# Kernel optimization log

Hardware: AMD Instinct MI355X
Metric: run time of the kernel (lower is better)

Reference implementation:

```python
import jax, jax.numpy as jnp
import numpy as np


def setup_inputs() -> dict:
    key = jax.random.key(0)
    k1, k2, k3 = jax.random.split(key, 3)
    B, N, D = 32, 1024, 256  # batch, seq len (shared), window_len
    t = jax.random.normal(k1, (B, N, D), dtype=jnp.float32)
    f = jax.random.normal(k2, (B, N, D), dtype=jnp.float32)
    W = jax.random.normal(k3, (D, D), dtype=jnp.float32)  # nn.init.normal_(std=1)
    return {"t": t, "f": f, "W": W}


def reference(t, f, W):
    # s_weight[b,n,m] = t[b,n,:] @ W @ f[b,m,:]
    tW = jnp.einsum('bnd,de->bne', t, W)          # [B,N,D]
    s_weight = jnp.einsum('bne,bme->bnm', tW, f)  # [B,N,N]
    t_weight = jax.nn.softmax(s_weight, axis=1)   # softmax over L_t (dim=1)
    f_weight = jax.nn.softmax(s_weight, axis=2)   # softmax over L_f (dim=2)
    # t_out = t^T @ t_weight -> [B,D,N]
    t_out = jnp.einsum('bnd,bnm->bdm', t, t_weight)
    # f_out = f^T @ f_weight -> [B,D,N] (requires L_t == L_f)
    f_out = jnp.einsum('bmd,bmk->bdk', f, f_weight)
    # Dropout(0.3) omitted (eval-mode identity) for deterministic reference.
    return (t_out, f_out)
```

## Files before the change

kernel.cpp:

```cpp
#include <hip/hip_runtime.h>
#include <math.h>

#define BB 32
#define NN 1024
#define DD 256
#define KSTEP 32
#define LDK 40

typedef __attribute__((ext_vector_type(8))) short short8;
typedef __attribute__((ext_vector_type(8))) unsigned short u16x8;
typedef __attribute__((ext_vector_type(4))) float f32x4;

__device__ __forceinline__ unsigned short f2bf(float x) {
  unsigned u = __float_as_uint(x);
  return (unsigned short)((u + 0x7fffu + ((u >> 16) & 1u)) >> 16);
}
__device__ __forceinline__ unsigned short f2bf_fast(float x) {
  return (unsigned short)((__float_as_uint(x) + 0x8000u) >> 16);
}
__device__ __forceinline__ float bf2f(unsigned short h) {
  return __uint_as_float((unsigned)h << 16);
}

__global__ __launch_bounds__(256) void k_split(const float* __restrict__ src,
                                               unsigned short* __restrict__ hi,
                                               unsigned short* __restrict__ lo, int n4) {
  int i = blockIdx.x * 256 + threadIdx.x;
  if (i >= n4) return;
  float4 v = ((const float4*)src)[i];
  float xs[4] = {v.x, v.y, v.z, v.w};
  ushort4 h4, l4;
  unsigned short* hp = (unsigned short*)&h4;
  unsigned short* lp = (unsigned short*)&l4;
  #pragma unroll
  for (int j = 0; j < 4; ++j) {
    unsigned short h = f2bf(xs[j]);
    hp[j] = h;
    lp[j] = f2bf(xs[j] - bf2f(h));
  }
  ((ushort4*)hi)[i] = h4;
  ((ushort4*)lo)[i] = l4;
}

__global__ __launch_bounds__(256) void k_splitW(const float* __restrict__ W,
                                                unsigned short* __restrict__ Wth,
                                                unsigned short* __restrict__ Wtl) {
  int k = blockIdx.x, n = threadIdx.x;
  float x = W[k * DD + n];
  unsigned short h = f2bf(x);
  Wth[n * DD + k] = h;
  Wtl[n * DD + k] = f2bf(x - bf2f(h));
}

__global__ __launch_bounds__(256) void k_transT(const unsigned short* __restrict__ in,
                                                unsigned short* __restrict__ out) {
  const int b = blockIdx.z;
  const int n0 = blockIdx.x * 64, d0 = blockIdx.y * 64;
  const int tid = threadIdx.x;
  const int nl = tid & 63, dc = tid >> 6;
  #pragma unroll
  for (int dj = 0; dj < 16; ++dj) {
    int d = d0 + dc * 16 + dj;
    unsigned short v = in[((size_t)b * NN + n0 + nl) * DD + d];
    out[((size_t)b * DD + d) * NN + n0 + nl] = v;
  }
}

template <int EPI>
__global__ __launch_bounds__(256) void k_gemm_nt(const unsigned short* __restrict__ Ahg,
                                                 const unsigned short* __restrict__ Alg,
                                                 const unsigned short* __restrict__ Bhg,
                                                 const unsigned short* __restrict__ Blg,
                                                 unsigned short* __restrict__ outh,
                                                 unsigned short* __restrict__ outl,
                                                 float* __restrict__ outf,
                                                 float2* __restrict__ prow,
                                                 float2* __restrict__ pcol, int b0) {
  size_t aoff = 0, boff = 0, coff = 0;
  const int g = blockIdx.z;
  if (EPI == 1) {
    int b = b0 + g;
    aoff = (size_t)b * NN * DD;
    boff = (size_t)b * NN * DD;
    coff = (size_t)g * NN * NN;
  }
  const int n0 = blockIdx.x * 128, m0 = blockIdx.y * 128;
  __shared__ unsigned short Ah[128][LDK], Al[128][LDK], Bh[128][LDK], Bl[128][LDK];
  const int tid = threadIdx.x;
  const int lane = tid & 63, w = tid >> 6;
  const int wr = (w >> 1) * 64, wc = (w & 1) * 64;
  const int sr = tid >> 1, sk = (tid & 1) * 16;

  f32x4 acc[4][4] = {};
  const int fr = lane & 15, fk = (lane >> 4) * 8;

  for (int k0 = 0; k0 < DD; k0 += KSTEP) {
    const size_t abase = aoff + (size_t)(n0 + sr) * DD + k0 + sk;
    const size_t bbase = boff + (size_t)(m0 + sr) * DD + k0 + sk;
    *(u16x8*)&Ah[sr][sk] = *(const u16x8*)&Ahg[abase];
    *(u16x8*)&Ah[sr][sk + 8] = *(const u16x8*)&Ahg[abase + 8];
    *(u16x8*)&Al[sr][sk] = *(const u16x8*)&Alg[abase];
    *(u16x8*)&Al[sr][sk + 8] = *(const u16x8*)&Alg[abase + 8];
    *(u16x8*)&Bh[sr][sk] = *(const u16x8*)&Bhg[bbase];
    *(u16x8*)&Bh[sr][sk + 8] = *(const u16x8*)&Bhg[bbase + 8];
    *(u16x8*)&Bl[sr][sk] = *(const u16x8*)&Blg[bbase];
    *(u16x8*)&Bl[sr][sk + 8] = *(const u16x8*)&Blg[bbase + 8];
    __syncthreads();
    short8 ah[4], al[4], bh[4], bl[4];
    #pragma unroll
    for (int mi = 0; mi < 4; ++mi) {
      ah[mi] = *(const short8*)&Ah[wr + mi * 16 + fr][fk];
      al[mi] = *(const short8*)&Al[wr + mi * 16 + fr][fk];
    }
    #pragma unroll
    for (int ni = 0; ni < 4; ++ni) {
      bh[ni] = *(const short8*)&Bh[wc + ni * 16 + fr][fk];
      bl[ni] = *(const short8*)&Bl[wc + ni * 16 + fr][fk];
    }
    #pragma unroll
    for (int mi = 0; mi < 4; ++mi)
      #pragma unroll
      for (int ni = 0; ni < 4; ++ni) {
        acc[mi][ni] = __builtin_amdgcn_mfma_f32_16x16x32_bf16(ah[mi], bh[ni], acc[mi][ni], 0, 0, 0);
        acc[mi][ni] = __builtin_amdgcn_mfma_f32_16x16x32_bf16(ah[mi], bl[ni], acc[mi][ni], 0, 0, 0);
        acc[mi][ni] = __builtin_amdgcn_mfma_f32_16x16x32_bf16(al[mi], bh[ni], acc[mi][ni], 0, 0, 0);
      }
    __syncthreads();
  }
  const int fq = (lane >> 4) * 4;
  if (EPI == 0) {
    #pragma unroll
    for (int mi = 0; mi < 4; ++mi)
      #pragma unroll
      for (int ni = 0; ni < 4; ++ni)
        #pragma unroll
        for (int q = 0; q < 4; ++q) {
          int row = n0 + wr + mi * 16 + fq + q;
          int col = m0 + wc + ni * 16 + fr;
          float x = acc[mi][ni][q];
          unsigned short h = f2bf(x);
          outh[(size_t)row * 256 + col] = h;
          outl[(size_t)row * 256 + col] = f2bf(x - bf2f(h));
        }
  } else {
    #pragma unroll
    for (int mi = 0; mi < 4; ++mi)
      #pragma unroll
      for (int ni = 0; ni < 4; ++ni) {
        int colm = m0 + wc + ni * 16 + fr;
        int nbase = n0 + wr + mi * 16 + fq;
        float4 v = {acc[mi][ni][0], acc[mi][ni][1], acc[mi][ni][2], acc[mi][ni][3]};
        *(float4*)&outf[coff + (size_t)colm * NN + nbase] = v;
      }
    float2 (*rowbuf)[2] = (float2(*)[2])&Ah[0][0];
    float2 (*colbuf)[2] = (float2(*)[2])&Bh[0][0];
    #pragma unroll
    for (int mi = 0; mi < 4; ++mi)
      #pragma unroll
      for (int q = 0; q < 4; ++q) {
        float v0 = acc[mi][0][q], v1 = acc[mi][1][q], v2 = acc[mi][2][q], v3 = acc[mi][3][q];
        float mx = fmaxf(fmaxf(v0, v1), fmaxf(v2, v3));
        #pragma unroll
        for (int mask = 1; mask <= 8; mask <<= 1) mx = fmaxf(mx, __shfl_xor(mx, mask));
        float se = __expf(v0 - mx) + __expf(v1 - mx) + __expf(v2 - mx) + __expf(v3 - mx);
        #pragma unroll
        for (int mask = 1; mask <= 8; mask <<= 1) se += __shfl_xor(se, mask);
        if (fr == 0) rowbuf[wr + mi * 16 + fq + q][w & 1] = make_float2(mx, se);
      }
    #pragma unroll
    for (int ni = 0; ni < 4; ++ni) {
      float mx = -INFINITY;
      #pragma unroll
      for (int mi = 0; mi < 4; ++mi)
        #pragma unroll
        for (int q = 0; q < 4; ++q) mx = fmaxf(mx, acc[mi][ni][q]);
      mx = fmaxf(mx, __shfl_xor(mx, 16));
      mx = fmaxf(mx, __shfl_xor(mx, 32));
      float se = 0.f;
      #pragma unroll
      for (int mi = 0; mi < 4; ++mi)
        #pragma unroll
        for (int q = 0; q < 4; ++q) se += __expf(acc[mi][ni][q] - mx);
      se += __shfl_xor(se, 16);
      se += __shfl_xor(se, 32);
      if ((lane >> 4) == 0) colbuf[wc + ni * 16 + fr][w >> 1] = make_float2(mx, se);
    }
    __syncthreads();
    if (tid < 128) {
      float2 a = rowbuf[tid][0], c = rowbuf[tid][1];
      float nm = fmaxf(a.x, c.x);
      float s = a.y * __expf(a.x - nm) + c.y * __expf(c.x - nm);
      prow[((size_t)g * NN + n0 + tid) * 8 + blockIdx.y] = make_float2(nm, s);
    } else {
      int m = tid - 128;
      float2 a = colbuf[m][0], c = colbuf[m][1];
      float nm = fmaxf(a.x, c.x);
      float s = a.y * __expf(a.x - nm) + c.y * __expf(c.x - nm);
      pcol[((size_t)g * NN + m0 + m) * 8 + blockIdx.x] = make_float2(nm, s);
    }
  }
}

__global__ __launch_bounds__(256) void k_comb(const float2* __restrict__ part,
                                              float* __restrict__ lse, int b0) {
  const int g = blockIdx.y, b = b0 + g;
  const int i = blockIdx.x * 256 + threadIdx.x;
  float mx = -INFINITY, sum = 0.f;
  #pragma unroll
  for (int c = 0; c < 8; ++c) {
    float2 p = part[((size_t)g * NN + i) * 8 + c];
    float nm = fmaxf(mx, p.x);
    sum = sum * __expf(mx - nm) + p.y * __expf(p.x - nm);
    mx = nm;
  }
  lse[(size_t)b * NN + i] = mx + __logf(sum);
}

__global__ __launch_bounds__(256) void k_outdual(const unsigned short* __restrict__ tTg,
                                                 const unsigned short* __restrict__ fTg,
                                                 const float* __restrict__ sT,
                                                 const float* __restrict__ lr,
                                                 const float* __restrict__ lc,
                                                 float* __restrict__ out_t,
                                                 float* __restrict__ out_f, int b0) {
  const int g = blockIdx.z, b = b0 + g;
  const int c0 = blockIdx.x * 64;
  const int d0 = blockIdx.y * 128;
  const unsigned short* At = tTg + (size_t)b * DD * NN;
  const unsigned short* Af = fTg + (size_t)b * DD * NN;
  const float* S = sT + (size_t)g * NN * NN;
  __shared__ unsigned short Ats[128][LDK], Afs[128][LDK];
  __shared__ unsigned short P1s[64][LDK], P2s[64][LDK];
  const int tid = threadIdx.x;
  const int lane = tid & 63, w = tid >> 6;
  const int wd = (w >> 1) * 64, wcc = (w & 1) * 32;
  const int fr = lane & 15, fk = (lane >> 4) * 8, fq = (lane >> 4) * 4;
  const int ar = tid >> 1, ak = (tid & 1) * 16;
  const int srow = tid >> 2, soff = (tid & 3) * 8;
  const float lcv = lc[(size_t)b * NN + c0 + srow];
  f32x4 acc1[4][2] = {}, acc2[4][2] = {};
  for (int r0 = 0; r0 < NN; r0 += KSTEP) {
    const size_t arow = (size_t)(d0 + ar) * NN + r0 + ak;
    u16x8 a_t0 = *(const u16x8*)&At[arow];
    u16x8 a_t1 = *(const u16x8*)&At[arow + 8];
    u16x8 a_f0 = *(const u16x8*)&Af[arow];
    u16x8 a_f1 = *(const u16x8*)&Af[arow + 8];
    float4 v0 = *(const float4*)&S[(size_t)(c0 + srow) * NN + r0 + soff];
    float4 v1 = *(const float4*)&S[(size_t)(c0 + srow) * NN + r0 + soff + 4];
    float4 l0 = *(const float4*)&lr[(size_t)b * NN + r0 + soff];
    float4 l1 = *(const float4*)&lr[(size_t)b * NN + r0 + soff + 4];
    float sv[8] = {v0.x, v0.y, v0.z, v0.w, v1.x, v1.y, v1.z, v1.w};
    float lv[8] = {l0.x, l0.y, l0.z, l0.w, l1.x, l1.y, l1.z, l1.w};
    u16x8 p1, p2;
    #pragma unroll
    for (int j = 0; j < 8; ++j) {
      p1[j] = f2bf_fast(__expf(sv[j] - lcv));
      p2[j] = f2bf_fast(__expf(sv[j] - lv[j]));
    }
    __syncthreads();
    *(u16x8*)&Ats[ar][ak] = a_t0;
    *(u16x8*)&Ats[ar][ak + 8] = a_t1;
    *(u16x8*)&Afs[ar][ak] = a_f0;
    *(u16x8*)&Afs[ar][ak + 8] = a_f1;
    *(u16x8*)&P1s[srow][soff] = p1;
    *(u16x8*)&P2s[srow][soff] = p2;
    __syncthreads();
    short8 at[4], af[4], b1[2], b2[2];
    #pragma unroll
    for (int mi = 0; mi < 4; ++mi) {
      at[mi] = *(const short8*)&Ats[wd + mi * 16 + fr][fk];
      af[mi] = *(const short8*)&Afs[wd + mi * 16 + fr][fk];
    }
    #pragma unroll
    for (int ci = 0; ci < 2; ++ci) {
      b1[ci] = *(const short8*)&P1s[wcc + ci * 16 + fr][fk];
      b2[ci] = *(const short8*)&P2s[wcc + ci * 16 + fr][fk];
    }
    #pragma unroll
    for (int mi = 0; mi < 4; ++mi)
      #pragma unroll
      for (int ci = 0; ci < 2; ++ci) {
        acc1[mi][ci] = __builtin_amdgcn_mfma_f32_16x16x32_bf16(at[mi], b1[ci], acc1[mi][ci], 0, 0, 0);
        acc2[mi][ci] = __builtin_amdgcn_mfma_f32_16x16x32_bf16(af[mi], b2[ci], acc2[mi][ci], 0, 0, 0);
      }
  }
  float* Ot = out_t + (size_t)b * DD * NN;
  float* Of = out_f + (size_t)b * DD * NN;
  #pragma unroll
  for (int mi = 0; mi < 4; ++mi)
    #pragma unroll
    for (int ci = 0; ci < 2; ++ci)
      #pragma unroll
      for (int q = 0; q < 4; ++q) {
        int d = d0 + wd + mi * 16 + fq + q;
        int c = c0 + wcc + ci * 16 + fr;
        Ot[(size_t)d * NN + c] = acc1[mi][ci][q];
        Of[(size_t)d * NN + c] = acc2[mi][ci][q];
      }
}

extern "C" void kernel_launch(void* const* d_in, const int* in_sizes, int n_in,
                              void* d_out, int out_size, void* d_ws, size_t ws_size,
                              hipStream_t stream) {
  const float* t = (const float*)d_in[0];
  const float* f = (const float*)d_in[1];
  const float* W = (const float*)d_in[2];
  float* out = (float*)d_out;

  const size_t NE = (size_t)BB * NN * DD;
  char* ws = (char*)d_ws;
  size_t off = 0;
  auto alloc = [&](size_t bytes) { char* p = ws + off; off += (bytes + 255) & ~(size_t)255; return p; };
  unsigned short* f_hi = (unsigned short*)alloc(NE * 2);
  unsigned short* f_lo = (unsigned short*)alloc(NE * 2);
  unsigned short* tw_hi = (unsigned short*)alloc(NE * 2);
  unsigned short* tw_lo = (unsigned short*)alloc(NE * 2);
  unsigned short* tT = (unsigned short*)alloc(NE * 2);
  unsigned short* fT = (unsigned short*)alloc(NE * 2);
  unsigned short* Wth = (unsigned short*)alloc((size_t)DD * DD * 2);
  unsigned short* Wtl = (unsigned short*)alloc((size_t)DD * DD * 2);
  float* lr = (float*)alloc((size_t)BB * NN * 4);
  float* lc = (float*)alloc((size_t)BB * NN * 4);
  float2* prow = (float2*)alloc((size_t)BB * NN * 8 * 8);
  float2* pcol = (float2*)alloc((size_t)BB * NN * 8 * 8);
  size_t fixed_bytes = off;
  float* sbuf = (float*)(ws + fixed_bytes);
  unsigned short* t_hi = (unsigned short*)(ws + fixed_bytes);
  unsigned short* t_lo = t_hi + NE;
  size_t per_batch = (size_t)NN * NN * 4;
  int G = 1;
  if (ws_size > fixed_bytes + per_batch) {
    size_t avail = (ws_size - fixed_bytes) / per_batch;
    G = (int)(avail < BB ? avail : BB);
    if (G < 1) G = 1;
  }

  float* out_t = out;
  float* out_f = out + (size_t)BB * DD * NN;

  k_split<<<(int)((NE / 4 + 255) / 256), 256, 0, stream>>>(t, t_hi, t_lo, (int)(NE / 4));
  k_split<<<(int)((NE / 4 + 255) / 256), 256, 0, stream>>>(f, f_hi, f_lo, (int)(NE / 4));
  k_splitW<<<DD, DD, 0, stream>>>(W, Wth, Wtl);
  k_transT<<<dim3(NN / 64, DD / 64, BB), 256, 0, stream>>>(t_hi, tT);
  k_transT<<<dim3(NN / 64, DD / 64, BB), 256, 0, stream>>>(f_hi, fT);
  k_gemm_nt<0><<<dim3(256, 2, 1), 256, 0, stream>>>(t_hi, t_lo, Wth, Wtl, tw_hi, tw_lo,
                                                    nullptr, nullptr, nullptr, 0);

  for (int b0 = 0; b0 < BB; b0 += G) {
    int g = BB - b0 < G ? BB - b0 : G;
    k_gemm_nt<1><<<dim3(8, 8, g), 256, 0, stream>>>(tw_hi, tw_lo, f_hi, f_lo, nullptr, nullptr,
                                                    sbuf, prow, pcol, b0);
    k_comb<<<dim3(NN / 256, g), 256, 0, stream>>>(prow, lr, b0);
    k_comb<<<dim3(NN / 256, g), 256, 0, stream>>>(pcol, lc, b0);
    k_outdual<<<dim3(NN / 64, DD / 128, g), 256, 0, stream>>>(tT, fT, sbuf, lr, lc,
                                                              out_t, out_f, b0);
  }
}
```

Measured before the change: 368.3 us.

## Move softmax stats to separate kernel and widen outdual column tile to 128

Removes the fused row/column max-sum epilogue from the score GEMM and adds a standalone k_stats kernel that rereads the fp32 score matrix in 64x64 tiles to produce 16 partials per row and column, combined by k_comb16. Separately, k_outdual's column tile doubles from 64 to 128, so each block computes a 128x128 output with twice the accumulators. That halves how often the t/f transposed operands are reloaded per score column. The cost is an extra full read of the score buffer and higher register pressure in k_outdual, which may lower occupancy.

```diff
diff --git a/kernel.cpp b/kernel.cpp
--- a/kernel.cpp
+++ b/kernel.cpp
@@ -73,9 +73,7 @@
                                                  const unsigned short* __restrict__ Blg,
                                                  unsigned short* __restrict__ outh,
                                                  unsigned short* __restrict__ outl,
-                                                 float* __restrict__ outf,
-                                                 float2* __restrict__ prow,
-                                                 float2* __restrict__ pcol, int b0) {
+                                                 float* __restrict__ outf, int b0) {
   size_t aoff = 0, boff = 0, coff = 0;
   const int g = blockIdx.z;
   if (EPI == 1) {
@@ -152,63 +150,70 @@
         float4 v = {acc[mi][ni][0], acc[mi][ni][1], acc[mi][ni][2], acc[mi][ni][3]};
         *(float4*)&outf[coff + (size_t)colm * NN + nbase] = v;
       }
-    float2 (*rowbuf)[2] = (float2(*)[2])&Ah[0][0];
-    float2 (*colbuf)[2] = (float2(*)[2])&Bh[0][0];
-    #pragma unroll
-    for (int mi = 0; mi < 4; ++mi)
-      #pragma unroll
-      for (int q = 0; q < 4; ++q) {
-        float v0 = acc[mi][0][q], v1 = acc[mi][1][q], v2 = acc[mi][2][q], v3 = acc[mi][3][q];
-        float mx = fmaxf(fmaxf(v0, v1), fmaxf(v2, v3));
-        #pragma unroll
-        for (int mask = 1; mask <= 8; mask <<= 1) mx = fmaxf(mx, __shfl_xor(mx, mask));
-        float se = __expf(v0 - mx) + __expf(v1 - mx) + __expf(v2 - mx) + __expf(v3 - mx);
-        #pragma unroll
-        for (int mask = 1; mask <= 8; mask <<= 1) se += __shfl_xor(se, mask);
-        if (fr == 0) rowbuf[wr + mi * 16 + fq + q][w & 1] = make_float2(mx, se);
-      }
-    #pragma unroll
-    for (int ni = 0; ni < 4; ++ni) {
-      float mx = -INFINITY;
-      #pragma unroll
-      for (int mi = 0; mi < 4; ++mi)
-        #pragma unroll
-        for (int q = 0; q < 4; ++q) mx = fmaxf(mx, acc[mi][ni][q]);
-      mx = fmaxf(mx, __shfl_xor(mx, 16));
-      mx = fmaxf(mx, __shfl_xor(mx, 32));
-      float se = 0.f;
-      #pragma unroll
-      for (int mi = 0; mi < 4; ++mi)
-        #pragma unroll
-        for (int q = 0; q < 4; ++q) se += __expf(acc[mi][ni][q] - mx);
-      se += __shfl_xor(se, 16);
-      se += __shfl_xor(se, 32);
-      if ((lane >> 4) == 0) colbuf[wc + ni * 16 + fr][w >> 1] = make_float2(mx, se);
-    }
-    __syncthreads();
-    if (tid < 128) {
-      float2 a = rowbuf[tid][0], c = rowbuf[tid][1];
-      float nm = fmaxf(a.x, c.x);
-      float s = a.y * __expf(a.x - nm) + c.y * __expf(c.x - nm);
-      prow[((size_t)g * NN + n0 + tid) * 8 + blockIdx.y] = make_float2(nm, s);
-    } else {
-      int m = tid - 128;
-      float2 a = colbuf[m][0], c = colbuf[m][1];
-      float nm = fmaxf(a.x, c.x);
-      float s = a.y * __expf(a.x - nm) + c.y * __expf(c.x - nm);
-      pcol[((size_t)g * NN + m0 + m) * 8 + blockIdx.x] = make_float2(nm, s);
-    }
-  }
-}
-
-__global__ __launch_bounds__(256) void k_comb(const float2* __restrict__ part,
-                                              float* __restrict__ lse, int b0) {
+  }
+}
+
+__global__ __launch_bounds__(256) void k_stats(const float* __restrict__ sT,
+                                               float2* __restrict__ prow,
+                                               float2* __restrict__ pcol) {
+  const int g = blockIdx.z;
+  const int c0 = blockIdx.x * 64, r0 = blockIdx.y * 64;
+  const float* S = sT + (size_t)g * NN * NN;
+  __shared__ float Ls[64][65];
+  const int tid = threadIdx.x;
+  const int row = tid >> 4, c4 = (tid & 15) * 4;
+  #pragma unroll
+  for (int rr = 0; rr < 4; ++rr) {
+    int c = row + rr * 16;
+    *(float4*)&Ls[c][c4] = *(const float4*)&S[(size_t)(c0 + c) * NN + r0 + c4];
+  }
+  __syncthreads();
+  {
+    const int c = tid >> 2, seg = (tid & 3) * 16;
+    float mx = -INFINITY;
+    #pragma unroll
+    for (int j = 0; j < 16; ++j) mx = fmaxf(mx, Ls[c][seg + j]);
+    float se = 0.f;
+    #pragma unroll
+    for (int j = 0; j < 16; ++j) se += __expf(Ls[c][seg + j] - mx);
+    #pragma unroll
+    for (int mask = 1; mask <= 2; mask <<= 1) {
+      float m2 = __shfl_xor(mx, mask), s2 = __shfl_xor(se, mask);
+      float nm = fmaxf(mx, m2);
+      se = se * __expf(mx - nm) + s2 * __expf(m2 - nm);
+      mx = nm;
+    }
+    if ((tid & 3) == 0)
+      pcol[((size_t)g * NN + c0 + c) * 16 + blockIdx.y] = make_float2(mx, se);
+  }
+  {
+    const int r = tid >> 2, seg = (tid & 3) * 16;
+    float mx = -INFINITY;
+    #pragma unroll
+    for (int j = 0; j < 16; ++j) mx = fmaxf(mx, Ls[seg + j][r]);
+    float se = 0.f;
+    #pragma unroll
+    for (int j = 0; j < 16; ++j) se += __expf(Ls[seg + j][r] - mx);
+    #pragma unroll
+    for (int mask = 1; mask <= 2; mask <<= 1) {
+      float m2 = __shfl_xor(mx, mask), s2 = __shfl_xor(se, mask);
+      float nm = fmaxf(mx, m2);
+      se = se * __expf(mx - nm) + s2 * __expf(m2 - nm);
+      mx = nm;
+    }
+    if ((tid & 3) == 0)
+      prow[((size_t)g * NN + r0 + r) * 16 + blockIdx.x] = make_float2(mx, se);
+  }
+}
+
+__global__ __launch_bounds__(256) void k_comb16(const float2* __restrict__ part,
+                                                float* __restrict__ lse, int b0) {
   const int g = blockIdx.y, b = b0 + g;
   const int i = blockIdx.x * 256 + threadIdx.x;
   float mx = -INFINITY, sum = 0.f;
   #pragma unroll
-  for (int c = 0; c < 8; ++c) {
-    float2 p = part[((size_t)g * NN + i) * 8 + c];
+  for (int c = 0; c < 16; ++c) {
+    float2 p = part[((size_t)g * NN + i) * 16 + c];
     float nm = fmaxf(mx, p.x);
     sum = sum * __expf(mx - nm) + p.y * __expf(p.x - nm);
     mx = nm;
@@ -224,62 +229,71 @@
                                                  float* __restrict__ out_t,
                                                  float* __restrict__ out_f, int b0) {
   const int g = blockIdx.z, b = b0 + g;
-  const int c0 = blockIdx.x * 64;
+  const int c0 = blockIdx.x * 128;
   const int d0 = blockIdx.y * 128;
   const unsigned short* At = tTg + (size_t)b * DD * NN;
   const unsigned short* Af = fTg + (size_t)b * DD * NN;
   const float* S = sT + (size_t)g * NN * NN;
   __shared__ unsigned short Ats[128][LDK], Afs[128][LDK];
-  __shared__ unsigned short P1s[64][LDK], P2s[64][LDK];
+  __shared__ unsigned short P1s[128][LDK], P2s[128][LDK];
   const int tid = threadIdx.x;
   const int lane = tid & 63, w = tid >> 6;
-  const int wd = (w >> 1) * 64, wcc = (w & 1) * 32;
+  const int wd = (w >> 1) * 64, wcc = (w & 1) * 64;
   const int fr = lane & 15, fk = (lane >> 4) * 8, fq = (lane >> 4) * 4;
   const int ar = tid >> 1, ak = (tid & 1) * 16;
-  const int srow = tid >> 2, soff = (tid & 3) * 8;
-  const float lcv = lc[(size_t)b * NN + c0 + srow];
-  f32x4 acc1[4][2] = {}, acc2[4][2] = {};
+  const float lcv = lc[(size_t)b * NN + c0 + ar];
+  f32x4 acc1[4][4] = {}, acc2[4][4] = {};
   for (int r0 = 0; r0 < NN; r0 += KSTEP) {
     const size_t arow = (size_t)(d0 + ar) * NN + r0 + ak;
     u16x8 a_t0 = *(const u16x8*)&At[arow];
     u16x8 a_t1 = *(const u16x8*)&At[arow + 8];
     u16x8 a_f0 = *(const u16x8*)&Af[arow];
     u16x8 a_f1 = *(const u16x8*)&Af[arow + 8];
-    float4 v0 = *(const float4*)&S[(size_t)(c0 + srow) * NN + r0 + soff];
-    float4 v1 = *(const float4*)&S[(size_t)(c0 + srow) * NN + r0 + soff + 4];
-    float4 l0 = *(const float4*)&lr[(size_t)b * NN + r0 + soff];
-    float4 l1 = *(const float4*)&lr[(size_t)b * NN + r0 + soff + 4];
-    float sv[8] = {v0.x, v0.y, v0.z, v0.w, v1.x, v1.y, v1.z, v1.w};
-    float lv[8] = {l0.x, l0.y, l0.z, l0.w, l1.x, l1.y, l1.z, l1.w};
-    u16x8 p1, p2;
+    float4 v0 = *(const float4*)&S[(size_t)(c0 + ar) * NN + r0 + ak];
+    float4 v1 = *(const float4*)&S[(size_t)(c0 + ar) * NN + r0 + ak + 4];
+    float4 v2 = *(const float4*)&S[(size_t)(c0 + ar) * NN + r0 + ak + 8];
+    float4 v3 = *(const float4*)&S[(size_t)(c0 + ar) * NN + r0 + ak + 12];
+    float4 l0 = *(const float4*)&lr[(size_t)b * NN + r0 + ak];
+    float4 l1 = *(const float4*)&lr[(size_t)b * NN + r0 + ak + 4];
+    float4 l2 = *(const float4*)&lr[(size_t)b * NN + r0 + ak + 8];
+    float4 l3 = *(const float4*)&lr[(size_t)b * NN + r0 + ak + 12];
+    float sv[16] = {v0.x, v0.y, v0.z, v0.w, v1.x, v1.y, v1.z, v1.w,
+                    v2.x, v2.y, v2.z, v2.w, v3.x, v3.y, v3.z, v3.w};
+    float lv[16] = {l0.x, l0.y, l0.z, l0.w, l1.x, l1.y, l1.z, l1.w,
+                    l2.x, l2.y, l2.z, l2.w, l3.x, l3.y, l3.z, l3.w};
+    u16x8 p1a, p1b, p2a, p2b;
     #pragma unroll
     for (int j = 0; j < 8; ++j) {
-      p1[j] = f2bf_fast(__expf(sv[j] - lcv));
-      p2[j] = f2bf_fast(__expf(sv[j] - lv[j]));
+      p1a[j] = f2bf_fast(__expf(sv[j] - lcv));
+      p2a[j] = f2bf_fast(__expf(sv[j] - lv[j]));
+      p1b[j] = f2bf_fast(__expf(sv[j + 8] - lcv));
+      p2b[j] = f2bf_fast(__expf(sv[j + 8] - lv[j + 8]));
     }
     __syncthreads();
     *(u16x8*)&Ats[ar][ak] = a_t0;
     *(u16x8*)&Ats[ar][ak + 8] = a_t1;
     *(u16x8*)&Afs[ar][ak] = a_f0;
     *(u16x8*)&Afs[ar][ak + 8] = a_f1;
-    *(u16x8*)&P1s[srow][soff] = p1;
-    *(u16x8*)&P2s[srow][soff] = p2;
+    *(u16x8*)&P1s[ar][ak] = p1a;
+    *(u16x8*)&P1s[ar][ak + 8] = p1b;
+    *(u16x8*)&P2s[ar][ak] = p2a;
+    *(u16x8*)&P2s[ar][ak + 8] = p2b;
     __syncthreads();
-    short8 at[4], af[4], b1[2], b2[2];
+    short8 at[4], af[4], b1[4], b2[4];
     #pragma unroll
     for (int mi = 0; mi < 4; ++mi) {
       at[mi] = *(const short8*)&Ats[wd + mi * 16 + fr][fk];
       af[mi] = *(const short8*)&Afs[wd + mi * 16 + fr][fk];
     }
     #pragma unroll
-    for (int ci = 0; ci < 2; ++ci) {
+    for (int ci = 0; ci < 4; ++ci) {
       b1[ci] = *(const short8*)&P1s[wcc + ci * 16 + fr][fk];
       b2[ci] = *(const short8*)&P2s[wcc + ci * 16 + fr][fk];
     }
     #pragma unroll
     for (int mi = 0; mi < 4; ++mi)
       #pragma unroll
-      for (int ci = 0; ci < 2; ++ci) {
+      for (int ci = 0; ci < 4; ++ci) {
         acc1[mi][ci] = __builtin_amdgcn_mfma_f32_16x16x32_bf16(at[mi], b1[ci], acc1[mi][ci], 0, 0, 0);
         acc2[mi][ci] = __builtin_amdgcn_mfma_f32_16x16x32_bf16(af[mi], b2[ci], acc2[mi][ci], 0, 0, 0);
       }
@@ -289,7 +303,7 @@
   #pragma unroll
   for (int mi = 0; mi < 4; ++mi)
     #pragma unroll
-    for (int ci = 0; ci < 2; ++ci)
+    for (int ci = 0; ci < 4; ++ci)
       #pragma unroll
       for (int q = 0; q < 4; ++q) {
         int d = d0 + wd + mi * 16 + fq + q;
@@ -321,8 +335,8 @@
   unsigned short* Wtl = (unsigned short*)alloc((size_t)DD * DD * 2);
   float* lr = (float*)alloc((size_t)BB * NN * 4);
   float* lc = (float*)alloc((size_t)BB * NN * 4);
-  float2* prow = (float2*)alloc((size_t)BB * NN * 8 * 8);
-  float2* pcol = (float2*)alloc((size_t)BB * NN * 8 * 8);
+  float2* prow = (float2*)alloc((size_t)BB * NN * 16 * 8);
+  float2* pcol = (float2*)alloc((size_t)BB * NN * 16 * 8);
   size_t fixed_bytes = off;
   float* sbuf = (float*)(ws + fixed_bytes);
   unsigned short* t_hi = (unsigned short*)(ws + fixed_bytes);
@@ -344,15 +358,16 @@
   k_transT<<<dim3(NN / 64, DD / 64, BB), 256, 0, stream>>>(t_hi, tT);
   k_transT<<<dim3(NN / 64, DD / 64, BB), 256, 0, stream>>>(f_hi, fT);
   k_gemm_nt<0><<<dim3(256, 2, 1), 256, 0, stream>>>(t_hi, t_lo, Wth, Wtl, tw_hi, tw_lo,
-                                                    nullptr, nullptr, nullptr, 0);
+                                                    nullptr, 0);
 
   for (int b0 = 0; b0 < BB; b0 += G) {
     int g = BB - b0 < G ? BB - b0 : G;
     k_gemm_nt<1><<<dim3(8, 8, g), 256, 0, stream>>>(tw_hi, tw_lo, f_hi, f_lo, nullptr, nullptr,
-                                                    sbuf, prow, pcol, b0);
-    k_comb<<<dim3(NN / 256, g), 256, 0, stream>>>(prow, lr, b0);
-    k_comb<<<dim3(NN / 256, g), 256, 0, stream>>>(pcol, lc, b0);
-    k_outdual<<<dim3(NN / 64, DD / 128, g), 256, 0, stream>>>(tT, fT, sbuf, lr, lc,
-                                                              out_t, out_f, b0);
-  }
-}
+                                                    sbuf, b0);
+    k_stats<<<dim3(16, 16, g), 256, 0, stream>>>(sbuf, prow, pcol);
+    k_comb16<<<dim3(NN / 256, g), 256, 0, stream>>>(prow, lr, b0);
+    k_comb16<<<dim3(NN / 256, g), 256, 0, stream>>>(pcol, lc, b0);
+    k_outdual<<<dim3(NN / 128, DD / 128, g), 256, 0, stream>>>(tT, fT, sbuf, lr, lc,
+                                                               out_t, out_f, b0);
+  }
+}
```

Result: no change. 362.2 us (-1.7%).
